# Optimization experiments

Measured on AMD Instinct MI355X. Metric: run time of the kernel, lower is better.

## Reference

```python
import jax, jax.numpy as jnp
import numpy as np

N_NODES = 50000
N_EDGES = 800000
IN_DIM = 256
OUT_DIM = 256


def setup_inputs() -> dict:
    key = jax.random.key(0)
    k_feat, k_src, k_dst, k_w0, k_w1, k_b = jax.random.split(key, 6)
    feat = jax.random.normal(k_feat, (N_NODES, IN_DIM), dtype=jnp.float32)
    src = jax.random.randint(k_src, (N_EDGES,), 0, N_NODES, dtype=jnp.int64)
    dst = jax.random.randint(k_dst, (N_EDGES,), 0, N_NODES, dtype=jnp.int64)
    # GraphConv weights (Glorot-ish scale) and biases
    W0 = jax.random.normal(k_w0, (IN_DIM, OUT_DIM), dtype=jnp.float32) / np.sqrt(IN_DIM)
    W1 = jax.random.normal(k_w1, (OUT_DIM, OUT_DIM), dtype=jnp.float32) / np.sqrt(OUT_DIM)
    b0 = jnp.zeros((OUT_DIM,), dtype=jnp.float32)
    b1 = jnp.zeros((OUT_DIM,), dtype=jnp.float32)
    # single shared nn.PReLU parameter (torch default init 0.25)
    prelu_a = jnp.asarray(0.25, dtype=jnp.float32)
    return {"feat": feat, "src": src, "dst": dst,
            "W0": W0, "b0": b0, "W1": W1, "b1": b1, "prelu_a": prelu_a}


def _prelu(x, a):
    return jnp.where(x >= 0, x, a * x)


def reference(feat, src, dst, W0, b0, W1, b1, prelu_a):
    N = feat.shape[0]
    ones = jnp.ones((src.shape[0],), dtype=feat.dtype)
    out_deg = jnp.zeros((N,), dtype=feat.dtype).at[src].add(ones)
    in_deg = jnp.zeros((N,), dtype=feat.dtype).at[dst].add(ones)
    # DGL norm='both': clamp degrees to >=1 before rsqrt
    norm_s = jax.lax.rsqrt(jnp.maximum(out_deg, 1.0))[:, None]  # [N,1]
    norm_d = jax.lax.rsqrt(jnp.maximum(in_deg, 1.0))[:, None]   # [N,1]

    def graph_conv(h, W, b):
        # h' = D_in^{-1/2} A (D_out^{-1/2} h) W + b
        msg = (h * norm_s)[src]                                   # [E, d]
        agg = jax.ops.segment_sum(msg, dst, num_segments=N)       # [N, d]
        return (agg * norm_d) @ W + b

    h = _prelu(graph_conv(feat, W0, b0), prelu_a)
    hg = jnp.sum(h, axis=0, keepdims=True)                        # SumPooling [1, d]
    h = _prelu(graph_conv(h, W1, b1), prelu_a)
    hg = jnp.concatenate([hg, jnp.sum(h, axis=0, keepdims=True)], axis=-1)
    return (h, hg)
```

## Files before the change

kernel.cpp:

```cpp
#include <hip/hip_runtime.h>
#include <stdint.h>

#define NN 50000
#define NE 800000
#define DIM 256

#define HB 128
#define HT 512
#define HALF 25000
#define HWORDS 12500

#define NSLICE 4
#define SCH 64
#define NPB 32
#define ECH 1024

#define GB ((NN + 31) / 32)

typedef __bf16 bf16x8 __attribute__((ext_vector_type(8)));
typedef float f32x4 __attribute__((ext_vector_type(4)));
typedef float f32x2 __attribute__((ext_vector_type(2)));
typedef unsigned u32x4 __attribute__((ext_vector_type(4)));
typedef int i32x4 __attribute__((ext_vector_type(4)));

__device__ __forceinline__ unsigned short f2bf(float f) {
  union { float f; unsigned u; } v; v.f = f;
  unsigned r = v.u + 0x7fffu + ((v.u >> 16) & 1u);
  return (unsigned short)(r >> 16);
}

__global__ __launch_bounds__(HT) void hist_kernel(const int* __restrict__ src,
                                                  const int* __restrict__ dst,
                                                  unsigned* __restrict__ Hs,
                                                  unsigned* __restrict__ Hd) {
  __shared__ unsigned lds[HALF];
  const int tid = threadIdx.x;
  const int b = blockIdx.x;
#pragma unroll
  for (int phase = 0; phase < 2; ++phase) {
    const int* arr = phase ? dst : src;
    unsigned* H = phase ? Hd : Hs;
    for (int w = tid; w < HALF; w += HT) lds[w] = 0u;
    __syncthreads();
    for (int e = b * HT + tid; e < NE; e += HB * HT) {
      unsigned n = (unsigned)arr[e];
      atomicAdd(&lds[n >> 1], 1u << ((n & 1) * 16));
    }
    __syncthreads();
    for (int w = tid; w < HALF; w += HT)
      H[(size_t)b * HALF + w] = lds[w];
    __syncthreads();
  }
}

__global__ void reduce_norm_kernel(const unsigned* __restrict__ Hs,
                                   const unsigned* __restrict__ Hd,
                                   unsigned* __restrict__ Pd,
                                   int* __restrict__ in_cnt,
                                   float* __restrict__ norm_s,
                                   float* __restrict__ norm_d,
                                   float* __restrict__ hg) {
  int w = blockIdx.x * blockDim.x + threadIdx.x;
  if (blockIdx.x == 0) {
    hg[threadIdx.x] = 0.f;
    hg[256 + threadIdx.x] = 0.f;
  }
  if (w >= 2 * HWORDS) return;
  unsigned ss = 0, dd = 0;
  for (int b = 0; b < HB; ++b) {
    Pd[(size_t)b * HALF + w] = dd;
    ss += Hs[(size_t)b * HALF + w];
    dd += Hd[(size_t)b * HALF + w];
  }
  int n0 = w * 2;
  unsigned s0 = ss & 0xffffu, s1 = ss >> 16;
  unsigned d0 = dd & 0xffffu, d1 = dd >> 16;
  in_cnt[n0] = (int)d0;
  in_cnt[n0 + 1] = (int)d1;
  norm_s[n0] = rsqrtf(fmaxf((float)s0, 1.0f));
  norm_s[n0 + 1] = rsqrtf(fmaxf((float)s1, 1.0f));
  norm_d[n0] = rsqrtf(fmaxf((float)d0, 1.0f));
  norm_d[n0 + 1] = rsqrtf(fmaxf((float)d1, 1.0f));
}

__global__ __launch_bounds__(1024) void scan_kernel(const int* __restrict__ in_cnt,
                                                    int* __restrict__ row_ptr) {
  __shared__ int wsum[16];
  int tid = threadIdx.x;
  int lane = tid & 63, wave = tid >> 6;
  int carry = 0;
  for (int base = 0; base < NN; base += 4096) {
    int i0 = base + tid * 4;
    int v[4];
#pragma unroll
    for (int j = 0; j < 4; ++j) {
      int i = i0 + j;
      v[j] = (i < NN) ? in_cnt[i] : 0;
    }
    int tsum = v[0] + v[1] + v[2] + v[3];
    int incl = tsum;
#pragma unroll
    for (int off = 1; off < 64; off <<= 1) {
      int t = __shfl_up(incl, off, 64);
      if (lane >= off) incl += t;
    }
    if (lane == 63) wsum[wave] = incl;
    __syncthreads();
    int waveoff = 0;
    for (int w = 0; w < wave; ++w) waveoff += wsum[w];
    int chunk_total = 0;
    for (int w = 0; w < 16; ++w) chunk_total += wsum[w];
    int run = carry + waveoff + (incl - tsum);
#pragma unroll
    for (int j = 0; j < 4; ++j) {
      int i = i0 + j;
      if (i < NN) row_ptr[i] = run;
      run += v[j];
    }
    carry += chunk_total;
    __syncthreads();
  }
  if (tid == 0) row_ptr[NN] = carry;
}

__global__ __launch_bounds__(HT) void fill_kernel(const int* __restrict__ src,
                                                  const int* __restrict__ dst,
                                                  const int* __restrict__ row_ptr,
                                                  const unsigned* __restrict__ Pd,
                                                  int* __restrict__ colx) {
  __shared__ unsigned lds[HALF];
  const int tid = threadIdx.x;
  const int b = blockIdx.x;
  for (int w = tid; w < HALF; w += HT) lds[w] = 0u;
  __syncthreads();
  for (int e = b * HT + tid; e < NE; e += HB * HT) {
    int n = dst[e];
    int sh = (n & 1) * 16;
    unsigned old = atomicAdd(&lds[n >> 1], 1u << sh);
    unsigned rank = (old >> sh) & 0xffffu;
    unsigned pref = (Pd[(size_t)b * HALF + (n >> 1)] >> sh) & 0xffffu;
    colx[row_ptr[n] + (int)pref + (int)rank] = src[e] << 7;
  }
}

__device__ __forceinline__ void swizzleW_body(const float* __restrict__ W,
                                              unsigned short* __restrict__ Wb, int idx) {
  int lane = idx & 63;
  int blk = idx >> 6;
  int kc = blk & 7, nt = blk >> 3;
  int kbase = kc * 32 + (lane >> 4) * 8;
  int col = nt * 16 + (lane & 15);
  ushort4 o0, o1;
  o0.x = f2bf(W[(size_t)(kbase + 0) * DIM + col]);
  o0.y = f2bf(W[(size_t)(kbase + 1) * DIM + col]);
  o0.z = f2bf(W[(size_t)(kbase + 2) * DIM + col]);
  o0.w = f2bf(W[(size_t)(kbase + 3) * DIM + col]);
  o1.x = f2bf(W[(size_t)(kbase + 4) * DIM + col]);
  o1.y = f2bf(W[(size_t)(kbase + 5) * DIM + col]);
  o1.z = f2bf(W[(size_t)(kbase + 6) * DIM + col]);
  o1.w = f2bf(W[(size_t)(kbase + 7) * DIM + col]);
  ((ushort4*)Wb)[idx * 2 + 0] = o0;
  ((ushort4*)Wb)[idx * 2 + 1] = o1;
}

__global__ void prep_kernel(const float* __restrict__ feat, const float* __restrict__ norm_s,
                            unsigned short* __restrict__ featb,
                            const float* __restrict__ W0, unsigned short* __restrict__ Wb0,
                            const float* __restrict__ W1, unsigned short* __restrict__ Wb1) {
  int blk = blockIdx.x;
  if (blk < 12500) {
    int i = blk * 256 + threadIdx.x;
    int node = i >> 6;
    int ch4 = i & 63;
    float s = norm_s[node];
    float4 v = ((const float4*)feat)[i];
    ushort4 o;
    o.x = f2bf(v.x * s); o.y = f2bf(v.y * s); o.z = f2bf(v.z * s); o.w = f2bf(v.w * s);
    int sl = ch4 >> 4;
    int w4 = ch4 & 15;
    ((ushort4*)featb)[(size_t)sl * (NN * 16) + (size_t)node * 16 + w4] = o;
  } else if (blk < 12532) {
    swizzleW_body(W0, Wb0, (blk - 12500) * 256 + threadIdx.x);
  } else {
    swizzleW_body(W1, Wb1, (blk - 12532) * 256 + threadIdx.x);
  }
}

__device__ __forceinline__ void acc_row(f32x2* a, u32x4 p) {
  f32x2 v0 = { __uint_as_float(p.x << 16), __uint_as_float(p.x & 0xffff0000u) };
  a[0] += v0;
  f32x2 v1 = { __uint_as_float(p.y << 16), __uint_as_float(p.y & 0xffff0000u) };
  a[1] += v1;
  f32x2 v2 = { __uint_as_float(p.z << 16), __uint_as_float(p.z & 0xffff0000u) };
  a[2] += v2;
  f32x2 v3 = { __uint_as_float(p.w << 16), __uint_as_float(p.w & 0xffff0000u) };
  a[3] += v3;
}

__global__ __launch_bounds__(256) void agg_kernel(const unsigned short* __restrict__ X,
                                                  unsigned short* __restrict__ agg,
                                                  const int* __restrict__ row_ptr,
                                                  const int* __restrict__ colx,
                                                  const float* __restrict__ norm_d) {
  __shared__ int ecol[ECH];
  const int s = blockIdx.x & (NSLICE - 1);
  const int nb = blockIdx.x >> 2;
  const int tid = threadIdx.x;
  const int grp = tid >> 3;
  const int cl = tid & 7;
  const int node = nb * NPB + grp;

  const int nfirst = nb * NPB;
  const int nlast = (nfirst + NPB < NN) ? (nfirst + NPB) : NN;
  const int estart = row_ptr[nfirst];
  const int eend = row_ptr[nlast];

  int e = 0, end = 0;
  if (node < NN) { e = row_ptr[node]; end = row_ptr[node + 1]; }

  const char* Xp = (const char*)(X + (size_t)s * (NN * SCH));
  const int lsub = cl * 16;

  f32x2 a[4];
#pragma unroll
  for (int j = 0; j < 4; ++j) a[j] = (f32x2){0.f, 0.f};

  const int base0 = estart & ~3;
  for (int base = base0; base < eend; base += ECH) {
    const int lim = (base + ECH < eend) ? (base + ECH) : eend;
    __syncthreads();
    for (int k = base + tid * 4; k < lim; k += 1024) {
      i32x4 v = __builtin_nontemporal_load((const i32x4*)(colx + k));
      *(i32x4*)&ecol[k - base] = v;
    }
    __syncthreads();
    const int hi = (end < lim) ? end : lim;
    for (; e + 8 <= hi; e += 8) {
      int o_[8];
#pragma unroll
      for (int j = 0; j < 8; ++j) o_[j] = ecol[e - base + j];
      u32x4 r_[8];
#pragma unroll
      for (int j = 0; j < 8; ++j)
        r_[j] = *(const u32x4*)(Xp + (size_t)(unsigned)(o_[j] | lsub));
#pragma unroll
      for (int j = 0; j < 8; ++j) acc_row(a, r_[j]);
    }
    if (e + 4 <= hi) {
      int o_[4];
#pragma unroll
      for (int j = 0; j < 4; ++j) o_[j] = ecol[e - base + j];
      u32x4 r_[4];
#pragma unroll
      for (int j = 0; j < 4; ++j)
        r_[j] = *(const u32x4*)(Xp + (size_t)(unsigned)(o_[j] | lsub));
#pragma unroll
      for (int j = 0; j < 4; ++j) acc_row(a, r_[j]);
      e += 4;
    }
    for (; e < hi; ++e) {
      int o0 = ecol[e - base];
      u32x4 r = *(const u32x4*)(Xp + (size_t)(unsigned)(o0 | lsub));
      acc_row(a, r);
    }
  }

  if (node < NN) {
    float nd = norm_d[node];
    u32x4 o;
    o.x = (unsigned)f2bf(a[0].x * nd) | ((unsigned)f2bf(a[0].y * nd) << 16);
    o.y = (unsigned)f2bf(a[1].x * nd) | ((unsigned)f2bf(a[1].y * nd) << 16);
    o.z = (unsigned)f2bf(a[2].x * nd) | ((unsigned)f2bf(a[2].y * nd) << 16);
    o.w = (unsigned)f2bf(a[3].x * nd) | ((unsigned)f2bf(a[3].y * nd) << 16);
    __builtin_nontemporal_store(o, (u32x4*)(agg + (size_t)node * DIM + (size_t)s * SCH + (size_t)cl * 8));
  }
}

#define LDSROW 264
#define FROW 260
__global__ __launch_bounds__(256) void gemm_mfma_kernel(const unsigned short* __restrict__ A,
                                                        const unsigned short* __restrict__ Wb,
                                                        const float* __restrict__ bias,
                                                        const float* __restrict__ prelu_a_ptr,
                                                        const float* __restrict__ norm_s,
                                                        float* __restrict__ C,
                                                        unsigned short* __restrict__ Cb,
                                                        float* __restrict__ hg_part) {
  __shared__ unsigned short As[32 * LDSROW];
  int tid = threadIdx.x;
  int r0 = blockIdx.x * 32;
#pragma unroll
  for (int p = 0; p < 4; ++p) {
    int idx = p * 256 + tid;
    int row = idx >> 5;
    int seg = idx & 31;
    int grow = r0 + row;
    ushort4 v0 = {0, 0, 0, 0}, v1 = {0, 0, 0, 0};
    if (grow < NN) {
      const ushort4* g = (const ushort4*)(A + (size_t)grow * DIM + seg * 8);
      v0 = g[0]; v1 = g[1];
    }
    *(ushort4*)(&As[row * LDSROW + seg * 8 + 0]) = v0;
    *(ushort4*)(&As[row * LDSROW + seg * 8 + 4]) = v1;
  }
  __syncthreads();

  int wave = tid >> 6, lane = tid & 63;
  int quad = lane >> 4, l16 = lane & 15;

  f32x4 acc[2][4];
#pragma unroll
  for (int mt = 0; mt < 2; ++mt)
#pragma unroll
    for (int nti = 0; nti < 4; ++nti)
      acc[mt][nti] = (f32x4){0.f, 0.f, 0.f, 0.f};

#pragma unroll
  for (int kc = 0; kc < 8; ++kc) {
    bf16x8 a[2], b[4];
#pragma unroll
    for (int mt = 0; mt < 2; ++mt)
      a[mt] = *(const bf16x8*)(&As[(mt * 16 + l16) * LDSROW + kc * 32 + quad * 8]);
#pragma unroll
    for (int nti = 0; nti < 4; ++nti) {
      int nt = wave * 4 + nti;
      b[nti] = *(const bf16x8*)(Wb + ((size_t)(nt * 8 + kc) * 64 + lane) * 8);
    }
#pragma unroll
    for (int mt = 0; mt < 2; ++mt)
#pragma unroll
      for (int nti = 0; nti < 4; ++nti)
        acc[mt][nti] = __builtin_amdgcn_mfma_f32_16x16x32_bf16(a[mt], b[nti], acc[mt][nti], 0, 0, 0);
  }

  float pa = *prelu_a_ptr;
  float bv[4], cs[4];
#pragma unroll
  for (int nti = 0; nti < 4; ++nti) {
    bv[nti] = bias[wave * 64 + nti * 16 + l16];
    cs[nti] = 0.f;
  }
#pragma unroll
  for (int mt = 0; mt < 2; ++mt) {
#pragma unroll
    for (int nti = 0; nti < 4; ++nti) {
#pragma unroll
      for (int r = 0; r < 4; ++r) {
        int rowg = r0 + mt * 16 + quad * 4 + r;
        float x = acc[mt][nti][r] + bv[nti];
        x = (x >= 0.f) ? x : pa * x;
        acc[mt][nti][r] = x;
        if (rowg < NN) cs[nti] += x;
      }
    }
  }
#pragma unroll
  for (int nti = 0; nti < 4; ++nti) {
    cs[nti] += __shfl_xor(cs[nti], 16, 64);
    cs[nti] += __shfl_xor(cs[nti], 32, 64);
  }
  if (quad == 0) {
#pragma unroll
    for (int nti = 0; nti < 4; ++nti)
      hg_part[(size_t)blockIdx.x * 256 + wave * 64 + nti * 16 + l16] = cs[nti];
  }

  float* LF = (float*)As;
#pragma unroll
  for (int chunk = 0; chunk < 2; ++chunk) {
    __syncthreads();
#pragma unroll
    for (int nti = 0; nti < 4; ++nti) {
      int colw = wave * 64 + nti * 16 + l16;
#pragma unroll
      for (int r = 0; r < 4; ++r)
        LF[(quad * 4 + r) * FROW + colw] = acc[chunk][nti][r];
    }
    __syncthreads();
    int rowbase = r0 + chunk * 16;
    if (C) {
#pragma unroll
      for (int s = 0; s < 4; ++s) {
        int g = s * 256 + tid;
        int row = g >> 6, cg = g & 63;
        int rowg = rowbase + row;
        if (rowg < NN) {
          float4 v = *(const float4*)&LF[row * FROW + cg * 4];
          *(float4*)(C + (size_t)rowg * DIM + cg * 4) = v;
        }
      }
    }
    if (Cb) {
#pragma unroll
      for (int s = 0; s < 2; ++s) {
        int g = s * 256 + tid;
        int row = g >> 5, cg = g & 31;
        int rowg = rowbase + row;
        if (rowg < NN) {
          float ns = norm_s[rowg];
          float4 v0 = *(const float4*)&LF[row * FROW + cg * 8];
          float4 v1 = *(const float4*)&LF[row * FROW + cg * 8 + 4];
          uint4 o;
          o.x = (unsigned)f2bf(v0.x * ns) | ((unsigned)f2bf(v0.y * ns) << 16);
          o.y = (unsigned)f2bf(v0.z * ns) | ((unsigned)f2bf(v0.w * ns) << 16);
          o.z = (unsigned)f2bf(v1.x * ns) | ((unsigned)f2bf(v1.y * ns) << 16);
          o.w = (unsigned)f2bf(v1.z * ns) | ((unsigned)f2bf(v1.w * ns) << 16);
          unsigned short* outp = Cb + (size_t)(cg >> 3) * (NN * SCH)
                               + (size_t)rowg * SCH + (size_t)(cg & 7) * 8;
          *(uint4*)outp = o;
        }
      }
    }
  }
}

__global__ __launch_bounds__(256) void hg_reduce_kernel(const float* __restrict__ hg_part,
                                                        float* __restrict__ hg) {
  const int layer = blockIdx.x >> 3;
  const int chunk = blockIdx.x & 7;
  const int c = threadIdx.x;
  const float* base = hg_part + (size_t)layer * GB * 256;
  const int per = (GB + 7) / 8;
  int b0 = chunk * per;
  int b1 = (b0 + per < GB) ? (b0 + per) : GB;
  float s0 = 0.f, s1 = 0.f, s2 = 0.f, s3 = 0.f;
  int b = b0;
  for (; b + 4 <= b1; b += 4) {
    s0 += base[(size_t)(b + 0) * 256 + c];
    s1 += base[(size_t)(b + 1) * 256 + c];
    s2 += base[(size_t)(b + 2) * 256 + c];
    s3 += base[(size_t)(b + 3) * 256 + c];
  }
  for (; b < b1; ++b) s0 += base[(size_t)b * 256 + c];
  atomicAdd(&hg[layer * 256 + c], (s0 + s1) + (s2 + s3));
}

extern "C" void kernel_launch(void* const* d_in, const int* in_sizes, int n_in,
                              void* d_out, int out_size, void* d_ws, size_t ws_size,
                              hipStream_t stream) {
  const float* feat = (const float*)d_in[0];
  const int* src    = (const int*)d_in[1];
  const int* dst    = (const int*)d_in[2];
  const float* W0   = (const float*)d_in[3];
  const float* b0   = (const float*)d_in[4];
  const float* W1   = (const float*)d_in[5];
  const float* b1   = (const float*)d_in[6];
  const float* pa   = (const float*)d_in[7];

  float* out_h = (float*)d_out;
  float* hg    = out_h + (size_t)NN * DIM;

  char* w = (char*)d_ws;
  int* in_cnt   = (int*)w;        w += (size_t)NN * 4;
  float* norm_s = (float*)w;      w += (size_t)NN * 4;
  float* norm_d = (float*)w;      w += (size_t)NN * 4;
  int* row_ptr  = (int*)w;        w += (size_t)(NN + 16) * 4;
  int* colx     = (int*)w;        w += (size_t)(NE + 4) * 4;
  unsigned short* Wb0 = (unsigned short*)w;  w += (size_t)DIM * DIM * 2;
  unsigned short* Wb1 = (unsigned short*)w;  w += (size_t)DIM * DIM * 2;
  float* hg_part = (float*)w;     w += (size_t)2 * GB * 256 * 4;
  uintptr_t ap = ((uintptr_t)w + 255) & ~(uintptr_t)255;
  unsigned short* featb = (unsigned short*)ap;
  unsigned short* aggb  = featb + (size_t)NN * DIM;
  unsigned* Hs = (unsigned*)featb;
  unsigned* Hd = Hs + (size_t)HB * HALF;
  unsigned* Pd = (unsigned*)aggb;

  const int agg_blocks = NSLICE * ((NN + NPB - 1) / NPB);

  hist_kernel<<<HB, HT, 0, stream>>>(src, dst, Hs, Hd);
  reduce_norm_kernel<<<(2 * HWORDS + 255) / 256, 256, 0, stream>>>(Hs, Hd, Pd, in_cnt,
                                                                   norm_s, norm_d, hg);
  prep_kernel<<<12564, 256, 0, stream>>>(feat, norm_s, featb, W0, Wb0, W1, Wb1);
  scan_kernel<<<1, 1024, 0, stream>>>(in_cnt, row_ptr);
  fill_kernel<<<HB, HT, 0, stream>>>(src, dst, row_ptr, Pd, colx);

  agg_kernel<<<agg_blocks, 256, 0, stream>>>(featb, aggb, row_ptr, colx, norm_d);
  gemm_mfma_kernel<<<GB, 256, 0, stream>>>(aggb, Wb0, b0, pa, norm_s,
                                           (float*)nullptr, featb, hg_part);

  agg_kernel<<<agg_blocks, 256, 0, stream>>>(featb, aggb, row_ptr, colx, norm_d);
  gemm_mfma_kernel<<<GB, 256, 0, stream>>>(aggb, Wb1, b1, pa, norm_s,
                                           out_h, (unsigned short*)nullptr, hg_part + (size_t)GB * 256);

  hg_reduce_kernel<<<16, 256, 0, stream>>>(hg_part, hg);
}
```

Baseline: 340.3 us.

## Split histogram phases across blocks, parallelize scan, enlarge GEMM row tile

The histogram kernel now launches twice as many blocks, with src and dst counted by separate blocks instead of sequentially in each block. The single-block row-pointer scan is replaced by a three-kernel multi-block scan (partial sums, mid scan, write). The GEMM tile grows from 32 to 64 rows per block, doubling MFMA work per block and reusing each loaded weight fragment across more rows. These raise parallelism in small serial kernels and cut weight reloads, at the cost of two extra launches, more LDS and registers per GEMM block, and fewer GEMM blocks.

After: 314.2 us. -7.7%, faster.

```diff
diff --git a/kernel.cpp b/kernel.cpp
--- a/kernel.cpp
+++ b/kernel.cpp
@@ -15,7 +15,10 @@
 #define NPB 32
 #define ECH 1024
 
-#define GB ((NN + 31) / 32)
+#define GR 64
+#define GB ((NN + GR - 1) / GR)
+
+#define SCB 49
 
 typedef __bf16 bf16x8 __attribute__((ext_vector_type(8)));
 typedef float f32x4 __attribute__((ext_vector_type(4)));
@@ -35,22 +38,19 @@
                                                   unsigned* __restrict__ Hd) {
   __shared__ unsigned lds[HALF];
   const int tid = threadIdx.x;
-  const int b = blockIdx.x;
-#pragma unroll
-  for (int phase = 0; phase < 2; ++phase) {
-    const int* arr = phase ? dst : src;
-    unsigned* H = phase ? Hd : Hs;
-    for (int w = tid; w < HALF; w += HT) lds[w] = 0u;
-    __syncthreads();
-    for (int e = b * HT + tid; e < NE; e += HB * HT) {
-      unsigned n = (unsigned)arr[e];
-      atomicAdd(&lds[n >> 1], 1u << ((n & 1) * 16));
-    }
-    __syncthreads();
-    for (int w = tid; w < HALF; w += HT)
-      H[(size_t)b * HALF + w] = lds[w];
-    __syncthreads();
-  }
+  const int phase = blockIdx.x >> 7;
+  const int b = blockIdx.x & (HB - 1);
+  const int* arr = phase ? dst : src;
+  unsigned* H = phase ? Hd : Hs;
+  for (int w = tid; w < HALF; w += HT) lds[w] = 0u;
+  __syncthreads();
+  for (int e = b * HT + tid; e < NE; e += HB * HT) {
+    unsigned n = (unsigned)arr[e];
+    atomicAdd(&lds[n >> 1], 1u << ((n & 1) * 16));
+  }
+  __syncthreads();
+  for (int w = tid; w < HALF; w += HT)
+    H[(size_t)b * HALF + w] = lds[w];
 }
 
 __global__ void reduce_norm_kernel(const unsigned* __restrict__ Hs,
@@ -83,44 +83,69 @@
   norm_d[n0 + 1] = rsqrtf(fmaxf((float)d1, 1.0f));
 }
 
-__global__ __launch_bounds__(1024) void scan_kernel(const int* __restrict__ in_cnt,
-                                                    int* __restrict__ row_ptr) {
-  __shared__ int wsum[16];
-  int tid = threadIdx.x;
-  int lane = tid & 63, wave = tid >> 6;
-  int carry = 0;
-  for (int base = 0; base < NN; base += 4096) {
-    int i0 = base + tid * 4;
-    int v[4];
-#pragma unroll
-    for (int j = 0; j < 4; ++j) {
-      int i = i0 + j;
-      v[j] = (i < NN) ? in_cnt[i] : 0;
-    }
-    int tsum = v[0] + v[1] + v[2] + v[3];
-    int incl = tsum;
-#pragma unroll
-    for (int off = 1; off < 64; off <<= 1) {
-      int t = __shfl_up(incl, off, 64);
-      if (lane >= off) incl += t;
-    }
-    if (lane == 63) wsum[wave] = incl;
-    __syncthreads();
-    int waveoff = 0;
-    for (int w = 0; w < wave; ++w) waveoff += wsum[w];
-    int chunk_total = 0;
-    for (int w = 0; w < 16; ++w) chunk_total += wsum[w];
-    int run = carry + waveoff + (incl - tsum);
-#pragma unroll
-    for (int j = 0; j < 4; ++j) {
-      int i = i0 + j;
-      if (i < NN) row_ptr[i] = run;
-      run += v[j];
-    }
-    carry += chunk_total;
-    __syncthreads();
-  }
-  if (tid == 0) row_ptr[NN] = carry;
+__global__ __launch_bounds__(256) void scan_part_kernel(const int* __restrict__ in_cnt,
+                                                        int* __restrict__ csum) {
+  __shared__ int ws[4];
+  int i0 = blockIdx.x * 1024 + threadIdx.x * 4;
+  int s = 0;
+#pragma unroll
+  for (int j = 0; j < 4; ++j) {
+    int i = i0 + j;
+    if (i < NN) s += in_cnt[i];
+  }
+  int lane = threadIdx.x & 63, wave = threadIdx.x >> 6;
+#pragma unroll
+  for (int off = 32; off; off >>= 1) s += __shfl_down(s, off, 64);
+  if (lane == 0) ws[wave] = s;
+  __syncthreads();
+  if (threadIdx.x == 0) csum[blockIdx.x] = ws[0] + ws[1] + ws[2] + ws[3];
+}
+
+__global__ __launch_bounds__(64) void scan_mid_kernel(const int* __restrict__ csum,
+                                                      int* __restrict__ coff,
+                                                      int* __restrict__ row_ptr) {
+  int lane = threadIdx.x;
+  int v = (lane < SCB) ? csum[lane] : 0;
+  int incl = v;
+#pragma unroll
+  for (int off = 1; off < 64; off <<= 1) {
+    int t = __shfl_up(incl, off, 64);
+    if (lane >= off) incl += t;
+  }
+  if (lane < SCB) coff[lane] = incl - v;
+  if (lane == SCB - 1) row_ptr[NN] = incl;
+}
+
+__global__ __launch_bounds__(256) void scan_write_kernel(const int* __restrict__ in_cnt,
+                                                         const int* __restrict__ coff,
+                                                         int* __restrict__ row_ptr) {
+  __shared__ int wsum[4];
+  int tid = threadIdx.x, lane = tid & 63, wave = tid >> 6;
+  int i0 = blockIdx.x * 1024 + tid * 4;
+  int v[4];
+#pragma unroll
+  for (int j = 0; j < 4; ++j) {
+    int i = i0 + j;
+    v[j] = (i < NN) ? in_cnt[i] : 0;
+  }
+  int tsum = v[0] + v[1] + v[2] + v[3];
+  int incl = tsum;
+#pragma unroll
+  for (int off = 1; off < 64; off <<= 1) {
+    int t = __shfl_up(incl, off, 64);
+    if (lane >= off) incl += t;
+  }
+  if (lane == 63) wsum[wave] = incl;
+  __syncthreads();
+  int woff = 0;
+  for (int w = 0; w < wave; ++w) woff += wsum[w];
+  int run = coff[blockIdx.x] + woff + (incl - tsum);
+#pragma unroll
+  for (int j = 0; j < 4; ++j) {
+    int i = i0 + j;
+    if (i < NN) row_ptr[i] = run;
+    run += v[j];
+  }
 }
 
 __global__ __launch_bounds__(HT) void fill_kernel(const int* __restrict__ src,
@@ -286,11 +311,11 @@
                                                         float* __restrict__ C,
                                                         unsigned short* __restrict__ Cb,
                                                         float* __restrict__ hg_part) {
-  __shared__ unsigned short As[32 * LDSROW];
+  __shared__ unsigned short As[GR * LDSROW];
   int tid = threadIdx.x;
-  int r0 = blockIdx.x * 32;
-#pragma unroll
-  for (int p = 0; p < 4; ++p) {
+  int r0 = blockIdx.x * GR;
+#pragma unroll
+  for (int p = 0; p < 8; ++p) {
     int idx = p * 256 + tid;
     int row = idx >> 5;
     int seg = idx & 31;
@@ -308,18 +333,18 @@
   int wave = tid >> 6, lane = tid & 63;
   int quad = lane >> 4, l16 = lane & 15;
 
-  f32x4 acc[2][4];
-#pragma unroll
-  for (int mt = 0; mt < 2; ++mt)
+  f32x4 acc[4][4];
+#pragma unroll
+  for (int mt = 0; mt < 4; ++mt)
 #pragma unroll
     for (int nti = 0; nti < 4; ++nti)
       acc[mt][nti] = (f32x4){0.f, 0.f, 0.f, 0.f};
 
 #pragma unroll
   for (int kc = 0; kc < 8; ++kc) {
-    bf16x8 a[2], b[4];
-#pragma unroll
-    for (int mt = 0; mt < 2; ++mt)
+    bf16x8 a[4], b[4];
+#pragma unroll
+    for (int mt = 0; mt < 4; ++mt)
       a[mt] = *(const bf16x8*)(&As[(mt * 16 + l16) * LDSROW + kc * 32 + quad * 8]);
 #pragma unroll
     for (int nti = 0; nti < 4; ++nti) {
@@ -327,7 +352,7 @@
       b[nti] = *(const bf16x8*)(Wb + ((size_t)(nt * 8 + kc) * 64 + lane) * 8);
     }
 #pragma unroll
-    for (int mt = 0; mt < 2; ++mt)
+    for (int mt = 0; mt < 4; ++mt)
 #pragma unroll
       for (int nti = 0; nti < 4; ++nti)
         acc[mt][nti] = __builtin_amdgcn_mfma_f32_16x16x32_bf16(a[mt], b[nti], acc[mt][nti], 0, 0, 0);
@@ -341,7 +366,7 @@
     cs[nti] = 0.f;
   }
 #pragma unroll
-  for (int mt = 0; mt < 2; ++mt) {
+  for (int mt = 0; mt < 4; ++mt) {
 #pragma unroll
     for (int nti = 0; nti < 4; ++nti) {
 #pragma unroll
@@ -367,7 +392,7 @@
 
   float* LF = (float*)As;
 #pragma unroll
-  for (int chunk = 0; chunk < 2; ++chunk) {
+  for (int chunk = 0; chunk < 4; ++chunk) {
     __syncthreads();
 #pragma unroll
     for (int nti = 0; nti < 4; ++nti) {
@@ -456,6 +481,8 @@
   float* norm_d = (float*)w;      w += (size_t)NN * 4;
   int* row_ptr  = (int*)w;        w += (size_t)(NN + 16) * 4;
   int* colx     = (int*)w;        w += (size_t)(NE + 4) * 4;
+  int* csum     = (int*)w;        w += 64 * 4;
+  int* coff     = (int*)w;        w += 64 * 4;
   unsigned short* Wb0 = (unsigned short*)w;  w += (size_t)DIM * DIM * 2;
   unsigned short* Wb1 = (unsigned short*)w;  w += (size_t)DIM * DIM * 2;
   float* hg_part = (float*)w;     w += (size_t)2 * GB * 256 * 4;
@@ -468,11 +495,13 @@
 
   const int agg_blocks = NSLICE * ((NN + NPB - 1) / NPB);
 
-  hist_kernel<<<HB, HT, 0, stream>>>(src, dst, Hs, Hd);
+  hist_kernel<<<2 * HB, HT, 0, stream>>>(src, dst, Hs, Hd);
   reduce_norm_kernel<<<(2 * HWORDS + 255) / 256, 256, 0, stream>>>(Hs, Hd, Pd, in_cnt,
                                                                    norm_s, norm_d, hg);
   prep_kernel<<<12564, 256, 0, stream>>>(feat, norm_s, featb, W0, Wb0, W1, Wb1);
-  scan_kernel<<<1, 1024, 0, stream>>>(in_cnt, row_ptr);
+  scan_part_kernel<<<SCB, 256, 0, stream>>>(in_cnt, csum);
+  scan_mid_kernel<<<1, 64, 0, stream>>>(csum, coff, row_ptr);
+  scan_write_kernel<<<SCB, 256, 0, stream>>>(in_cnt, coff, row_ptr);
   fill_kernel<<<HB, HT, 0, stream>>>(src, dst, row_ptr, Pd, colx);
 
   agg_kernel<<<agg_blocks, 256, 0, stream>>>(featb, aggb, row_ptr, colx, norm_d);
```
